# Kernel tuning notes

Measured on AMD Instinct MI355X. Metric: run time of the kernel, lower is better.

Reference implementation:

```python
import jax, jax.numpy as jnp
import numpy as np

B, T, C = 2, 2048, 1024
NH, LAT, DHR = 16, 512, 64
DK = C // NH  # 64


def _rope(x, d):
    # interleaved RoPE as in source: freq = t+1, theta per pair repeated twice
    Tx = x.shape[1]
    freq = jnp.arange(Tx, dtype=jnp.float32)[:, None] + 1.0            # [T,1]
    pos = jnp.arange(d // 2, dtype=jnp.float32)[:, None]
    pos = jnp.repeat(pos, 2, axis=-1).reshape(1, -1)                   # [1,d] -> p0,p0,p1,p1,...
    theta = jnp.exp(-2.0 * pos / d * jnp.log(10000.0))
    cos = jnp.cos(freq * theta)                                        # [T,d]
    sin = jnp.sin(freq * theta)
    x32 = x.astype(jnp.float32)
    x1 = x32[..., 0::2]
    x2 = x32[..., 1::2]
    xrot = jnp.stack([-x2, x1], axis=-1).reshape(x32.shape)
    return (x32 * cos + xrot * sin).astype(x.dtype)


def setup_inputs() -> dict:
    key = jax.random.key(0)
    ks = jax.random.split(key, 13)
    s = lambda k, sh, fan: jax.random.normal(k, sh, jnp.float32) / np.sqrt(fan)
    return {
        'x': jax.random.normal(ks[0], (B, T, C), jnp.float32),
        'w1': s(ks[1], (C, 2 * LAT), C), 'b1': jnp.zeros((2 * LAT,), jnp.float32),
        'wkr': s(ks[2], (2 * LAT, DHR), 2 * LAT), 'bkr': jnp.zeros((DHR,), jnp.float32),
        'wqr': s(ks[3], (2 * LAT, DHR * NH), 2 * LAT), 'bqr': jnp.zeros((DHR * NH,), jnp.float32),
        'wkv': s(ks[4], (LAT, 2 * C), LAT), 'bkv': jnp.zeros((2 * C,), jnp.float32),
        'wq': s(ks[5], (LAT, C), LAT), 'bq': jnp.zeros((C,), jnp.float32),
        'wo': s(ks[6], (C, C), C), 'bo': jnp.zeros((C,), jnp.float32),
    }


def reference(x, w1, b1, wkr, bkr, wqr, bqr, wkv, bkv, wq, bq, wo, bo):
    h = x @ w1 + b1                           # [B,T,2*LAT]
    cKV, cq = jnp.split(h, 2, axis=-1)        # each [B,T,LAT]

    kRt = _rope(h @ wkr + bkr, DHR)           # [B,T,DHR]
    qRt = _rope(h @ wqr + bqr, DHR * NH)      # [B,T,NH*DHR]
    qRt = qRt.reshape(B, T, NH, DHR).transpose(0, 2, 1, 3)  # [B,NH,T,DHR]

    kv = cKV @ wkv + bkv                      # [B,T,2C]
    k, v = jnp.split(kv, 2, axis=-1)
    q = cq @ wq + bq                          # [B,T,C]

    to_heads = lambda t: t.reshape(B, T, NH, DK).transpose(0, 2, 1, 3)
    q, k, v = to_heads(q), to_heads(k), to_heads(v)   # [B,NH,T,DK]

    q = jnp.concatenate([q, qRt], axis=-1)                              # [B,NH,T,DK+DHR]
    kR = jnp.broadcast_to(kRt[:, None, :, :], (B, NH, T, DHR))
    k = jnp.concatenate([k, kR], axis=-1)                               # [B,NH,T,DK+DHR]

    dk = q.shape[-1]
    qf, kf, vf = q.astype(jnp.float32), k.astype(jnp.float32), v.astype(jnp.float32)
    w = jnp.einsum('bnTd,bntd->bnTt', qf, kf) * dk ** (-0.5)            # [B,NH,T,T]
    mask = jnp.tril(jnp.ones((T, T), jnp.float32))
    w = jnp.where(mask == 0, -jnp.inf, w)
    w = jax.nn.softmax(w, axis=-1)
    out = jnp.einsum('bnTt,bntd->bnTd', w, vf).astype(x.dtype)          # [B,NH,T,DK]

    out = out.transpose(0, 2, 1, 3).reshape(B, T, C)
    return out @ wo + bo
```

## Files before the change

### kernel.cpp

```cpp
#include <hip/hip_runtime.h>
#include <math.h>
#include <stdint.h>

#define B_   2
#define T_   2048
#define C_   1024
#define NH_  16
#define LAT_ 512
#define DHR_ 64
#define M_   (B_*T_)

typedef unsigned short u16;
typedef unsigned int u32;
typedef short short8 __attribute__((ext_vector_type(8)));
typedef short short4v __attribute__((ext_vector_type(4)));
typedef float f32x4 __attribute__((ext_vector_type(4)));

#define SCALE2 0.12752455489626498f

__device__ __forceinline__ u16 f2bf(float f) {
    union { float f; unsigned u; } x; x.f = f;
    unsigned r = x.u + 0x7fffu + ((x.u >> 16) & 1u);
    return (u16)(r >> 16);
}
__device__ __forceinline__ float bf2f(u16 v) {
    union { unsigned u; float f; } x; x.u = ((unsigned)v) << 16;
    return x.f;
}
__device__ __forceinline__ u32 asu32(float f) {
    union { float f; u32 u; } x; x.f = f; return x.u;
}
__device__ __forceinline__ u32 pack_bf2(float lo, float hi) {
    u32 a = asu32(lo) + 0x8000u;
    u32 b = asu32(hi) + 0x8000u;
    return __builtin_amdgcn_perm(b, a, 0x07060302u);
}

__device__ __forceinline__ void gl_lds16(const void* g, void* l) {
    auto* gp = reinterpret_cast<const __attribute__((address_space(1))) unsigned*>(
        reinterpret_cast<uintptr_t>(g));
    auto* lp = reinterpret_cast<__attribute__((address_space(3))) unsigned*>(
        reinterpret_cast<uintptr_t>(l));
    __builtin_amdgcn_global_load_lds(gp, lp, 16, 0, 0);
}

__device__ __forceinline__ void tr_tile(const float* __restrict__ W,
                                        u16* __restrict__ Wt,
                                        int K, int N, int bx, int by, int tid,
                                        float (*t)[33])
{
    const int tx = tid & 31;
    const int ty = tid >> 5;
    const int n0 = bx << 5;
    const int k0 = by << 5;
    #pragma unroll
    for (int r = 0; r < 4; ++r) {
        int row = ty + (r << 3);
        t[row][tx] = W[(size_t)(k0 + row) * N + n0 + tx];
    }
    __syncthreads();
    #pragma unroll
    for (int r = 0; r < 4; ++r) {
        int row = ty + (r << 3);
        Wt[(size_t)(n0 + row) * K + k0 + tx] = f2bf(t[tx][row]);
    }
}

__global__ __launch_bounds__(256)
void prep_all(const float* __restrict__ x, u16* __restrict__ xb,
              const float* __restrict__ w1,  const float* __restrict__ wqr,
              const float* __restrict__ wkr, const float* __restrict__ wkv,
              const float* __restrict__ wq,  const float* __restrict__ wo,
              u16* __restrict__ w1t,  u16* __restrict__ wqkt,
              u16* __restrict__ wkvt, u16* __restrict__ wqt,
              u16* __restrict__ wot,
              const float* __restrict__ bqr, const float* __restrict__ bkr,
              float* __restrict__ bqk)
{
    __shared__ float t[32][33];
    int id = blockIdx.x;
    const int tid = threadIdx.x;
    if (id < 4096) {
        int i = id * 256 + tid;
        float4 v = ((const float4*)x)[i];
        short4v s;
        s[0] = f2bf(v.x); s[1] = f2bf(v.y); s[2] = f2bf(v.z); s[3] = f2bf(v.w);
        ((short4v*)xb)[i] = s;
        return;
    }
    id -= 4096;
    if (id < 1024)      { tr_tile(w1,  w1t,  1024, 1024, id % 32, id / 32, tid, t); return; }
    id -= 1024;
    if (id < 1024)      { tr_tile(wqr, wqkt, 1024, 1024, id % 32, id / 32, tid, t); return; }
    id -= 1024;
    if (id < 64)        { tr_tile(wkr, wqkt + 1024 * 1024, 1024, 64, id % 2, id / 2, tid, t); return; }
    id -= 64;
    if (id < 1024)      { tr_tile(wkv, wkvt, 512, 2048, id % 64, id / 64, tid, t); return; }
    id -= 1024;
    if (id < 512)       { tr_tile(wq,  wqt,  512, 1024, id % 32, id / 32, tid, t); return; }
    id -= 512;
    if (id < 1024)      { tr_tile(wo,  wot,  1024, 1024, id % 32, id / 32, tid, t); return; }
    for (int i = tid; i < 1152; i += 256) {
        float v;
        if (i < 1024)      v = bqr[i];
        else if (i < 1088) v = bkr[i - 1024];
        else               v = 0.f;
        bqk[i] = v;
    }
}

template<int BM, int BN>
__device__ __forceinline__ void gemm_body(
    u16* __restrict__ AsB, u16* __restrict__ BsB,
    const u16* __restrict__ A, int lda,
    const u16* __restrict__ Bt, const float* __restrict__ bias,
    void* __restrict__ Out, bool outf32, float oscale,
    int N, int K, int m0, int n0, int tid)
{
    constexpr int MI = BM / 32;
    constexpr int NI = BN / 32;
    const int lane = tid & 63;
    const int ln   = lane & 15;
    const int quad = lane >> 4;
    const int wv   = tid >> 6;
    const int wm   = (wv & 1) * (BM / 2);
    const int wn   = (wv >> 1) * (BN / 2);

    f32x4 acc[MI][NI];
    #pragma unroll
    for (int i = 0; i < MI; ++i)
        #pragma unroll
        for (int j = 0; j < NI; ++j) acc[i][j] = (f32x4){0.f, 0.f, 0.f, 0.f};

    auto stage = [&](int bufi, int k0) {
        u16* As = AsB + bufi * (BM * 32);
        u16* Bs = BsB + bufi * (BN * 32);
        #pragma unroll
        for (int it = 0; it < BM / 64; ++it) {
            int flat = it * 256 + tid;
            gl_lds16(A + (size_t)(m0 + (flat >> 2)) * lda + k0 + ((flat & 3) << 3),
                     &As[flat * 8]);
        }
        #pragma unroll
        for (int it = 0; it < BN / 64; ++it) {
            int flat = it * 256 + tid;
            gl_lds16(Bt + (size_t)(n0 + (flat >> 2)) * K + k0 + ((flat & 3) << 3),
                     &Bs[flat * 8]);
        }
    };

    stage(0, 0);
    __syncthreads();

    int buf = 0;
    for (int k0 = 0; k0 < K; k0 += 32) {
        if (k0 + 32 < K) stage(buf ^ 1, k0 + 32);

        u16* As = AsB + buf * (BM * 32);
        u16* Bs = BsB + buf * (BN * 32);
        short8 af[MI], bfv[NI];
        #pragma unroll
        for (int mi = 0; mi < MI; ++mi)
            af[mi] = *(const short8*)(&As[(wm + mi * 16 + ln) * 32 + quad * 8]);
        #pragma unroll
        for (int ni = 0; ni < NI; ++ni)
            bfv[ni] = *(const short8*)(&Bs[(wn + ni * 16 + ln) * 32 + quad * 8]);
        #pragma unroll
        for (int mi = 0; mi < MI; ++mi)
            #pragma unroll
            for (int ni = 0; ni < NI; ++ni)
                acc[mi][ni] = __builtin_amdgcn_mfma_f32_16x16x32_bf16(af[mi], bfv[ni], acc[mi][ni], 0, 0, 0);

        __syncthreads();
        buf ^= 1;
    }

    float bb[NI];
    #pragma unroll
    for (int ni = 0; ni < NI; ++ni) bb[ni] = bias[n0 + wn + ni * 16 + ln];

    #pragma unroll
    for (int mi = 0; mi < MI; ++mi) {
        #pragma unroll
        for (int r = 0; r < 4; ++r) {
            const size_t row = (size_t)(m0 + wm + mi * 16 + quad * 4 + r);
            #pragma unroll
            for (int ni = 0; ni < NI; ++ni) {
                float v = (acc[mi][ni][r] + bb[ni]) * oscale;
                const size_t idx = row * N + n0 + wn + ni * 16 + ln;
                if (outf32) ((float*)Out)[idx] = v;
                else        ((u16*)Out)[idx]  = f2bf(v);
            }
        }
    }
}

template<int BM, int BN, bool OUTF32>
__global__ __launch_bounds__(256, 4)
void gemm_mfma(const u16* __restrict__ A, int lda,
               const u16* __restrict__ Bt,
               const float* __restrict__ bias,
               void* __restrict__ Out, int N, int K, float oscale)
{
    __shared__ __align__(16) u16 As[2 * BM * 32];
    __shared__ __align__(16) u16 Bs[2 * BN * 32];
    gemm_body<BM, BN>(As, Bs, A, lda, Bt, bias, Out, OUTF32, oscale,
                      N, K, blockIdx.y * BM, blockIdx.x * BN, threadIdx.x);
}

__global__ __launch_bounds__(256, 4)
void gemm3(const u16* __restrict__ hb,
           const u16* __restrict__ wqkt, const float* __restrict__ bqk, u16* __restrict__ Zqk,
           const u16* __restrict__ wkvt, const float* __restrict__ bkv, u16* __restrict__ kvbb,
           const u16* __restrict__ wqt,  const float* __restrict__ bq,  u16* __restrict__ qb)
{
    __shared__ __align__(16) u16 As[2 * 4096];
    __shared__ __align__(16) u16 Bs[2 * 4096];
    int id = blockIdx.x;
    const u16* A; const u16* Bt; const float* bias; u16* Out; int N, K, bx, by;
    float osc = 1.0f;
    if (id < 288)      { A = hb;       Bt = wqkt; bias = bqk; Out = Zqk;  N = 1152; K = 1024; bx = id % 9;  by = id / 9; }
    else if (id < 800) { id -= 288; A = hb;       Bt = wkvt; bias = bkv; Out = kvbb; N = 2048; K = 512;  bx = id % 16; by = id / 16; }
    else               { id -= 800; A = hb + 512; Bt = wqt;  bias = bq;  Out = qb;   N = 1024; K = 512;  bx = id % 8;  by = id / 8; osc = SCALE2; }
    gemm_body<128, 128>(As, Bs, A, 1024, Bt, bias, Out, false, osc, N, K,
                        by * 128, bx * 128, threadIdx.x);
}

__global__ void rope_bf(u16* __restrict__ Zqk)
{
    int idx = blockIdx.x * 256 + threadIdx.x;
    u16* p;
    int t;
    float e, osc;
    if (idx < M_ * 512) {
        int row = idx >> 9, pr = idx & 511;
        e = (-2.0f * (float)pr / 1024.0f) * 9.210340371976184f;
        p = Zqk + (size_t)row * 1152 + (pr << 1);
        t = row & (T_ - 1);
        osc = SCALE2;
    } else {
        int r = idx - M_ * 512;
        if (r >= M_ * 32) return;
        int row = r >> 5, pr = r & 31;
        e = (-2.0f * (float)pr / 64.0f) * 9.210340371976184f;
        p = Zqk + 1024 + (size_t)row * 1152 + (pr << 1);
        t = row & (T_ - 1);
        osc = 1.0f;
    }
    float theta = expf(e);
    float ang = (float)(t + 1) * theta;
    float s = sinf(ang), c = cosf(ang);
    float x1 = bf2f(p[0]);
    float x2 = bf2f(p[1]);
    p[0] = f2bf((x1 * c - x2 * s) * osc);
    p[1] = f2bf((x2 * c + x1 * s) * osc);
}

__global__ __launch_bounds__(256)
void reshape_kv(const u16* __restrict__ kvb,
                const u16* __restrict__ kR, int kRstride,
                u16* __restrict__ Kf,
                u16* __restrict__ Vt)
{
    __shared__ u16 t[64 * 68];
    const int tid = threadIdx.x;
    const int bh  = blockIdx.y;
    const int kt  = blockIdx.x;
    const int b = bh >> 4, h = bh & 15;
    const int bT = b * T_;
    const int k0 = kt << 6;

    #pragma unroll
    for (int it = 0; it < 4; ++it) {
        int flat = it * 256 + tid;
        int j = flat >> 4;
        int g = flat & 15;
        int gl = g ^ (j & 7);
        const u16* src = (g < 8)
            ? (kvb + (size_t)(bT + k0 + j) * 2048 + h * 64 + ((gl & 7) << 3))
            : (kR  + (size_t)(bT + k0 + j) * kRstride + ((gl & 7) << 3));
        *(short8*)(Kf + ((size_t)bh * 2048 + k0 + j) * 128 + (g << 3)) = *(const short8*)src;
    }
    #pragma unroll
    for (int it = 0; it < 2; ++it) {
        int flat = it * 256 + tid;
        int j  = flat >> 3;
        int d8 = (flat & 7) << 3;
        *(short8*)(&t[j * 68 + d8]) =
            *(const short8*)(kvb + (size_t)(bT + k0 + j) * 2048 + 1024 + h * 64 + d8);
    }
    __syncthreads();
    #pragma unroll
    for (int it = 0; it < 2; ++it) {
        int flat = it * 256 + tid;
        int dv = flat >> 3;
        int p  = flat & 7;
        int gl = p ^ (dv & 7);
        short8 v;
        #pragma unroll
        for (int e = 0; e < 8; ++e) v[e] = (short)t[(gl * 8 + e) * 68 + dv];
        *(short8*)(Vt + (size_t)bh * 131072 + (size_t)dv * 2048 + k0 + (p << 3)) = v;
    }
}

__global__ __launch_bounds__(256, 2)
void attn_mfma(const u16* __restrict__ qh,
               const u16* __restrict__ qR, int qRstride,
               const u16* __restrict__ Kf,
               const u16* __restrict__ Vtg,
               u16* __restrict__ Opart,
               float* __restrict__ Lpart)
{
    __shared__ __align__(16) u16 Ks[2][64 * 128];
    __shared__ __align__(16) u16 Vt[2][64 * 64];
    __shared__ __align__(16) u16 Ps[4 * 32 * 64];

    const int tid  = threadIdx.x;
    const int lane = tid & 63;
    const int ln   = lane & 15;
    const int quad = lane >> 4;
    const int wv   = tid >> 6;
    const int bh   = blockIdx.y;
    const int b    = bh >> 4;
    const int h    = bh & 15;
    const int bT   = b * T_;
    const int p    = blockIdx.x & 7;
    const int s    = blockIdx.x >> 3;
    const int ln7  = ln & 7;

    auto stage = [&](int bufi, int kt) {
        const u16* ksrc = Kf + ((size_t)bh * 2048 + (kt << 6)) * 128;
        #pragma unroll
        for (int it = 0; it < 4; ++it) {
            int flat = it * 256 + tid;
            gl_lds16(ksrc + flat * 8, &Ks[bufi][flat * 8]);
        }
        const u16* vsrc = Vtg + (size_t)bh * 131072 + (kt << 6);
        #pragma unroll
        for (int it = 0; it < 2; ++it) {
            int flat = it * 256 + tid;
            gl_lds16(vsrc + (size_t)(flat >> 3) * 2048 + ((flat & 7) << 3),
                     &Vt[bufi][flat * 8]);
        }
    };

    const int qts[2]    = { p, 15 - p };
    const int halves[2] = { s, 1 - s };

    for (int seg = 0; seg < 2; ++seg) {
        const int qt   = qts[seg];
        const int hf   = halves[seg];
        const int n    = 2 * qt + 2;
        const int ktlo = hf ? (n >> 1) : 0;
        const int kthi = hf ? n : (n >> 1);
        const int part = ((bh * 16 + qt) << 1) + hf;
        const int wq0  = qt * 128 + wv * 32;

        short8 aq[2][4];
        #pragma unroll
        for (int ni = 0; ni < 2; ++ni) {
            const size_t row = (size_t)(bT + wq0 + ni * 16 + ln);
            #pragma unroll
            for (int kk = 0; kk < 4; ++kk) {
                const int col = kk * 32 + quad * 8;
                const u16* src = (kk < 2)
                    ? (qh + row * C_ + h * 64 + col)
                    : (qR + row * qRstride + h * 64 + (col - 64));
                aq[ni][kk] = *(const short8*)src;
            }
        }

        f32x4 O[2][4];
        float l_lane[2] = { 0.f, 0.f };
        #pragma unroll
        for (int ni = 0; ni < 2; ++ni)
            #pragma unroll
            for (int mt = 0; mt < 4; ++mt) O[ni][mt] = (f32x4){0.f, 0.f, 0.f, 0.f};

        stage(0, ktlo);
        __syncthreads();

        for (int kt = ktlo; kt < kthi; ++kt) {
            const int cur = (kt - ktlo) & 1;
            if (kt + 1 < kthi) stage(cur ^ 1, kt + 1);

            const int k0 = kt << 6;
            if (k0 <= wq0 + 31) {
                f32x4 S[2][4];
                #pragma unroll
                for (int ni = 0; ni < 2; ++ni)
                    #pragma unroll
                    for (int mi = 0; mi < 4; ++mi)
                        S[ni][mi] = (f32x4){0.f, 0.f, 0.f, 0.f};

                #pragma unroll
                for (int kk = 0; kk < 4; ++kk) {
                    #pragma unroll
                    for (int mi = 0; mi < 4; ++mi) {
                        short8 ak = *(const short8*)(
                            &Ks[cur][(mi * 16 + ln) * 128 + (((kk * 4 + quad) ^ ln7) << 3)]);
                        S[0][mi] = __builtin_amdgcn_mfma_f32_16x16x32_bf16(ak, aq[0][kk], S[0][mi], 0, 0, 0);
                        S[1][mi] = __builtin_amdgcn_mfma_f32_16x16x32_bf16(ak, aq[1][kk], S[1][mi], 0, 0, 0);
                    }
                }

                const bool full = (k0 + 63) <= wq0;

                #pragma unroll
                for (int ni = 0; ni < 2; ++ni) {
                    const int qg = wq0 + ni * 16 + ln;
                    float ll = 0.f;
                    #pragma unroll
                    for (int mi = 0; mi < 4; ++mi) {
                        float pv[4];
                        #pragma unroll
                        for (int r = 0; r < 4; ++r) {
                            float sc = S[ni][mi][r];
                            if (!full) {
                                int key = k0 + mi * 16 + quad * 4 + r;
                                if (key > qg) sc = -1e30f;
                            }
                            pv[r] = __builtin_amdgcn_exp2f(sc);
                        }
                        ll += (pv[0] + pv[1]) + (pv[2] + pv[3]);
                        u32 pk0 = pack_bf2(pv[0], pv[1]);
                        u32 pk1 = pack_bf2(pv[2], pv[3]);
                        u32* dst = (u32*)&Ps[(wv * 32 + ni * 16 + ln) * 64 +
                                             (((mi * 2 + (quad >> 1)) ^ ln7) << 3) +
                                             ((quad & 1) << 2)];
                        dst[0] = pk0;
                        dst[1] = pk1;
                    }
                    l_lane[ni] += ll;
                }

                asm volatile("s_waitcnt lgkmcnt(0)" ::: "memory");

                #pragma unroll
                for (int c = 0; c < 2; ++c) {
                    const int pos = ((c * 4 + quad) ^ ln7) << 3;
                    short8 pb0 = *(const short8*)(&Ps[(wv * 32 +  0 + ln) * 64 + pos]);
                    short8 pb1 = *(const short8*)(&Ps[(wv * 32 + 16 + ln) * 64 + pos]);
                    #pragma unroll
                    for (int mt = 0; mt < 4; ++mt) {
                        short8 av = *(const short8*)(&Vt[cur][(mt * 16 + ln) * 64 + pos]);
                        O[0][mt] = __builtin_amdgcn_mfma_f32_16x16x32_bf16(av, pb0, O[0][mt], 0, 0, 0);
                        O[1][mt] = __builtin_amdgcn_mfma_f32_16x16x32_bf16(av, pb1, O[1][mt], 0, 0, 0);
                    }
                }
            }
            __syncthreads();
        }

        #pragma unroll
        for (int ni = 0; ni < 2; ++ni) {
            float l = l_lane[ni];
            l += __shfl_xor(l, 16);
            l += __shfl_xor(l, 32);
            const int qlocal = wv * 32 + ni * 16 + ln;
            u16* dst = Opart + ((size_t)part * 128 + qlocal) * 64;
            #pragma unroll
            for (int mt = 0; mt < 4; ++mt) {
                short4v o;
                o[0] = (short)f2bf(O[ni][mt][0]);
                o[1] = (short)f2bf(O[ni][mt][1]);
                o[2] = (short)f2bf(O[ni][mt][2]);
                o[3] = (short)f2bf(O[ni][mt][3]);
                *(short4v*)(dst + mt * 16 + quad * 4) = o;
            }
            if (quad == 0)
                Lpart[part * 128 + qlocal] = l;
            l_lane[ni] = 0.f;
        }
    }
}

__global__ void attn_merge(const u16* __restrict__ Opart,
                           const float* __restrict__ Lpart,
                           u16* __restrict__ out)
{
    int g = blockIdx.x * 256 + threadIdx.x;
    int row    = g >> 4;
    int c4     = (g & 15) << 2;
    int bhqt   = row >> 7;
    int qlocal = row & 127;
    float l0 = Lpart[(bhqt << 1) * 128 + qlocal];
    float l1 = Lpart[((bhqt << 1) + 1) * 128 + qlocal];
    float inv = 1.0f / (l0 + l1);
    short4v s0 = *(const short4v*)(Opart + ((size_t)(bhqt << 1) * 128 + qlocal) * 64 + c4);
    short4v s1 = *(const short4v*)(Opart + ((size_t)((bhqt << 1) + 1) * 128 + qlocal) * 64 + c4);
    int bh = bhqt >> 4, qt = bhqt & 15;
    int b = bh >> 4, h = bh & 15;
    size_t orow = (size_t)(b * T_ + qt * 128 + qlocal);
    short4v o;
    o[0] = (short)f2bf((bf2f((u16)s0[0]) + bf2f((u16)s1[0])) * inv);
    o[1] = (short)f2bf((bf2f((u16)s0[1]) + bf2f((u16)s1[1])) * inv);
    o[2] = (short)f2bf((bf2f((u16)s0[2]) + bf2f((u16)s1[2])) * inv);
    o[3] = (short)f2bf((bf2f((u16)s0[3]) + bf2f((u16)s1[3])) * inv);
    *(short4v*)(out + orow * C_ + h * 64 + c4) = o;
}

extern "C" void kernel_launch(void* const* d_in, const int* in_sizes, int n_in,
                              void* d_out, int out_size, void* d_ws, size_t ws_size,
                              hipStream_t stream)
{
    const float* x   = (const float*)d_in[0];
    const float* w1  = (const float*)d_in[1];
    const float* b1  = (const float*)d_in[2];
    const float* wkr = (const float*)d_in[3];
    const float* bkr = (const float*)d_in[4];
    const float* wqr = (const float*)d_in[5];
    const float* bqr = (const float*)d_in[6];
    const float* wkv = (const float*)d_in[7];
    const float* bkv = (const float*)d_in[8];
    const float* wq  = (const float*)d_in[9];
    const float* bq  = (const float*)d_in[10];
    const float* wo  = (const float*)d_in[11];
    const float* bo  = (const float*)d_in[12];
    float* out = (float*)d_out;

    u16* ws    = (u16*)d_ws;
    u16* buf0  = ws;
    u16* buf1  = buf0 + 4194304;
    u16* Zqk   = buf1 + 4194304;
    u16* kvbb  = Zqk  + 4718592;
    u16* w1t   = kvbb + 8388608;
    u16* wqkt  = w1t  + 1048576;
    u16* wkvt  = wqkt + 1179648;
    u16* wqt   = wkvt + 1048576;
    u16* wot   = wqt  + 524288;
    float* bqk = (float*)(wot + 1048576);
    u16* Kf    = (u16*)(bqk + 1280);
    u16* Vtg   = Kf  + 8388608;
    u16* Opart = Vtg + 4194304;
    float* Lprt = (float*)(Opart + 8388608);

    u16* xb    = buf0;
    u16* qb    = buf0;
    u16* hb    = buf1;
    u16* attnb = buf1;

    dim3 blk(256);

    prep_all<<<8769, blk, 0, stream>>>(x, xb, w1, wqr, wkr, wkv, wq, wo,
                                       w1t, wqkt, wkvt, wqt, wot,
                                       bqr, bkr, bqk);

    gemm_mfma<128, 64, false><<<dim3(16, 32), blk, 0, stream>>>(xb, 1024, w1t, b1, hb, 1024, 1024, 1.0f);
    gemm3<<<1056, blk, 0, stream>>>(hb, wqkt, bqk, Zqk, wkvt, bkv, kvbb, wqt, bq, qb);
    rope_bf<<<(M_ * 544 + 255) / 256, blk, 0, stream>>>(Zqk);
    reshape_kv<<<dim3(32, 32), blk, 0, stream>>>(kvbb, Zqk + 1024, 1152, Kf, Vtg);
    attn_mfma<<<dim3(16, 32), blk, 0, stream>>>(qb, Zqk, 1152, Kf, Vtg, Opart, Lprt);
    attn_merge<<<4096, blk, 0, stream>>>(Opart, Lprt, attnb);
    gemm_mfma<128, 64, true><<<dim3(16, 32), blk, 0, stream>>>(attnb, 1024, wot, bo, out, 1024, 1024, 1.0f);
}
```

Baseline: 240.8 us.

## Split attention key range into thirds and single-buffer K/V tiles

```diff
diff --git a/kernel.cpp b/kernel.cpp
--- a/kernel.cpp
+++ b/kernel.cpp
@@ -196,7 +196,7 @@
 }
 
 template<int BM, int BN, bool OUTF32>
-__global__ __launch_bounds__(256, 4)
+__global__ __launch_bounds__(256, 3)
 void gemm_mfma(const u16* __restrict__ A, int lda,
                const u16* __restrict__ Bt,
                const float* __restrict__ bias,
@@ -208,7 +208,7 @@
                       N, K, blockIdx.y * BM, blockIdx.x * BN, threadIdx.x);
 }
 
-__global__ __launch_bounds__(256, 4)
+__global__ __launch_bounds__(256, 3)
 void gemm3(const u16* __restrict__ hb,
            const u16* __restrict__ wqkt, const float* __restrict__ bqk, u16* __restrict__ Zqk,
            const u16* __restrict__ wkvt, const float* __restrict__ bkv, u16* __restrict__ kvbb,
@@ -303,7 +303,7 @@
     }
 }
 
-__global__ __launch_bounds__(256, 2)
+__global__ __launch_bounds__(256, 3)
 void attn_mfma(const u16* __restrict__ qh,
                const u16* __restrict__ qR, int qRstride,
                const u16* __restrict__ Kf,
@@ -311,8 +311,8 @@
                u16* __restrict__ Opart,
                float* __restrict__ Lpart)
 {
-    __shared__ __align__(16) u16 Ks[2][64 * 128];
-    __shared__ __align__(16) u16 Vt[2][64 * 64];
+    __shared__ __align__(16) u16 Ks[64 * 128];
+    __shared__ __align__(16) u16 Vt[64 * 64];
     __shared__ __align__(16) u16 Ps[4 * 32 * 64];
 
     const int tid  = threadIdx.x;
@@ -324,51 +324,37 @@
     const int b    = bh >> 4;
     const int h    = bh & 15;
     const int bT   = b * T_;
-    const int p    = blockIdx.x & 7;
-    const int s    = blockIdx.x >> 3;
+    const int p    = blockIdx.x / 3;
+    const int a    = blockIdx.x % 3;
     const int ln7  = ln & 7;
 
-    auto stage = [&](int bufi, int kt) {
+    auto stage = [&](int kt) {
         const u16* ksrc = Kf + ((size_t)bh * 2048 + (kt << 6)) * 128;
         #pragma unroll
         for (int it = 0; it < 4; ++it) {
             int flat = it * 256 + tid;
-            gl_lds16(ksrc + flat * 8, &Ks[bufi][flat * 8]);
+            gl_lds16(ksrc + flat * 8, &Ks[flat * 8]);
         }
         const u16* vsrc = Vtg + (size_t)bh * 131072 + (kt << 6);
         #pragma unroll
         for (int it = 0; it < 2; ++it) {
             int flat = it * 256 + tid;
             gl_lds16(vsrc + (size_t)(flat >> 3) * 2048 + ((flat & 7) << 3),
-                     &Vt[bufi][flat * 8]);
+                     &Vt[flat * 8]);
         }
     };
 
     const int qts[2]    = { p, 15 - p };
-    const int halves[2] = { s, 1 - s };
+    const int thirds[2] = { a, 2 - a };
 
     for (int seg = 0; seg < 2; ++seg) {
         const int qt   = qts[seg];
-        const int hf   = halves[seg];
+        const int th   = thirds[seg];
         const int n    = 2 * qt + 2;
-        const int ktlo = hf ? (n >> 1) : 0;
-        const int kthi = hf ? n : (n >> 1);
-        const int part = ((bh * 16 + qt) << 1) + hf;
+        const int ktlo = th * n / 3;
+        const int kthi = (th + 1) * n / 3;
+        const int part = (bh * 16 + qt) * 3 + th;
         const int wq0  = qt * 128 + wv * 32;
-
-        short8 aq[2][4];
-        #pragma unroll
-        for (int ni = 0; ni < 2; ++ni) {
-            const size_t row = (size_t)(bT + wq0 + ni * 16 + ln);
-            #pragma unroll
-            for (int kk = 0; kk < 4; ++kk) {
-                const int col = kk * 32 + quad * 8;
-                const u16* src = (kk < 2)
-                    ? (qh + row * C_ + h * 64 + col)
-                    : (qR + row * qRstride + h * 64 + (col - 64));
-                aq[ni][kk] = *(const short8*)src;
-            }
-        }
 
         f32x4 O[2][4];
         float l_lane[2] = { 0.f, 0.f };
@@ -377,79 +363,92 @@
             #pragma unroll
             for (int mt = 0; mt < 4; ++mt) O[ni][mt] = (f32x4){0.f, 0.f, 0.f, 0.f};
 
-        stage(0, ktlo);
-        __syncthreads();
-
-        for (int kt = ktlo; kt < kthi; ++kt) {
-            const int cur = (kt - ktlo) & 1;
-            if (kt + 1 < kthi) stage(cur ^ 1, kt + 1);
-
-            const int k0 = kt << 6;
-            if (k0 <= wq0 + 31) {
-                f32x4 S[2][4];
-                #pragma unroll
-                for (int ni = 0; ni < 2; ++ni)
-                    #pragma unroll
-                    for (int mi = 0; mi < 4; ++mi)
-                        S[ni][mi] = (f32x4){0.f, 0.f, 0.f, 0.f};
-
+        if (ktlo < kthi) {
+            short8 aq[2][4];
+            #pragma unroll
+            for (int ni = 0; ni < 2; ++ni) {
+                const size_t row = (size_t)(bT + wq0 + ni * 16 + ln);
                 #pragma unroll
                 for (int kk = 0; kk < 4; ++kk) {
+                    const int col = kk * 32 + quad * 8;
+                    const u16* src = (kk < 2)
+                        ? (qh + row * C_ + h * 64 + col)
+                        : (qR + row * qRstride + h * 64 + (col - 64));
+                    aq[ni][kk] = *(const short8*)src;
+                }
+            }
+
+            for (int kt = ktlo; kt < kthi; ++kt) {
+                __syncthreads();
+                stage(kt);
+                __syncthreads();
+
+                const int k0 = kt << 6;
+                if (k0 <= wq0 + 31) {
+                    f32x4 S[2][4];
                     #pragma unroll
-                    for (int mi = 0; mi < 4; ++mi) {
-                        short8 ak = *(const short8*)(
-                            &Ks[cur][(mi * 16 + ln) * 128 + (((kk * 4 + quad) ^ ln7) << 3)]);
-                        S[0][mi] = __builtin_amdgcn_mfma_f32_16x16x32_bf16(ak, aq[0][kk], S[0][mi], 0, 0, 0);
-                        S[1][mi] = __builtin_amdgcn_mfma_f32_16x16x32_bf16(ak, aq[1][kk], S[1][mi], 0, 0, 0);
+                    for (int ni = 0; ni < 2; ++ni)
+                        #pragma unroll
+                        for (int mi = 0; mi < 4; ++mi)
+                            S[ni][mi] = (f32x4){0.f, 0.f, 0.f, 0.f};
+
+                    #pragma unroll
+                    for (int kk = 0; kk < 4; ++kk) {
+                        #pragma unroll
+                        for (int mi = 0; mi < 4; ++mi) {
+                            short8 ak = *(const short8*)(
+                                &Ks[(mi * 16 + ln) * 128 + (((kk * 4 + quad) ^ ln7) << 3)]);
+                            S[0][mi] = __builtin_amdgcn_mfma_f32_16x16x32_bf16(ak, aq[0][kk], S[0][mi], 0, 0, 0);
+                            S[1][mi] = __builtin_amdgcn_mfma_f32_16x16x32_bf16(ak, aq[1][kk], S[1][mi], 0, 0, 0);
+                        }
                     }
-                }
-
-                const bool full = (k0 + 63) <= wq0;
-
-                #pragma unroll
-                for (int ni = 0; ni < 2; ++ni) {
-                    const int qg = wq0 + ni * 16 + ln;
-                    float ll = 0.f;
+
+                    const bool full = (k0 + 63) <= wq0;
+
                     #pragma unroll
-                    for (int mi = 0; mi < 4; ++mi) {
-                        float pv[4];
+                    for (int ni = 0; ni < 2; ++ni) {
+                        const int qg = wq0 + ni * 16 + ln;
+                        float ll = 0.f;
                         #pragma unroll
-                        for (int r = 0; r < 4; ++r) {
-                            float sc = S[ni][mi][r];
-                            if (!full) {
-                                int key = k0 + mi * 16 + quad * 4 + r;
-                                if (key > qg) sc = -1e30f;
+                        for (int mi = 0; mi < 4; ++mi) {
+                            float pv[4];
+                            #pragma unroll
+                            for (int r = 0; r < 4; ++r) {
+                                float sc = S[ni][mi][r];
+                                if (!full) {
+                                    int key = k0 + mi * 16 + quad * 4 + r;
+                                    if (key > qg) sc = -1e30f;
+                                }
+                                pv[r] = __builtin_amdgcn_exp2f(sc);
                             }
-                            pv[r] = __builtin_amdgcn_exp2f(sc);
+                            ll += (pv[0] + pv[1]) + (pv[2] + pv[3]);
+                            u32 pk0 = pack_bf2(pv[0], pv[1]);
+                            u32 pk1 = pack_bf2(pv[2], pv[3]);
+                            u32* dst = (u32*)&Ps[(wv * 32 + ni * 16 + ln) * 64 +
+                                                 (((mi * 2 + (quad >> 1)) ^ ln7) << 3) +
+                                                 ((quad & 1) << 2)];
+                            dst[0] = pk0;
+                            dst[1] = pk1;
                         }
-                        ll += (pv[0] + pv[1]) + (pv[2] + pv[3]);
-                        u32 pk0 = pack_bf2(pv[0], pv[1]);
-                        u32 pk1 = pack_bf2(pv[2], pv[3]);
-                        u32* dst = (u32*)&Ps[(wv * 32 + ni * 16 + ln) * 64 +
-                                             (((mi * 2 + (quad >> 1)) ^ ln7) << 3) +
-                                             ((quad & 1) << 2)];
-                        dst[0] = pk0;
-                        dst[1] = pk1;
+                        l_lane[ni] += ll;
                     }
-                    l_lane[ni] += ll;
-                }
-
-                asm volatile("s_waitcnt lgkmcnt(0)" ::: "memory");
-
-                #pragma unroll
-                for (int c = 0; c < 2; ++c) {
-                    const int pos = ((c * 4 + quad) ^ ln7) << 3;
-                    short8 pb0 = *(const short8*)(&Ps[(wv * 32 +  0 + ln) * 64 + pos]);
-                    short8 pb1 = *(const short8*)(&Ps[(wv * 32 + 16 + ln) * 64 + pos]);
+
+                    asm volatile("s_waitcnt lgkmcnt(0)" ::: "memory");
+
                     #pragma unroll
-                    for (int mt = 0; mt < 4; ++mt) {
-                        short8 av = *(const short8*)(&Vt[cur][(mt * 16 + ln) * 64 + pos]);
-                        O[0][mt] = __builtin_amdgcn_mfma_f32_16x16x32_bf16(av, pb0, O[0][mt], 0, 0, 0);
-                        O[1][mt] = __builtin_amdgcn_mfma_f32_16x16x32_bf16(av, pb1, O[1][mt], 0, 0, 0);
+                    for (int c = 0; c < 2; ++c) {
+                        const int pos = ((c * 4 + quad) ^ ln7) << 3;
+                        short8 pb0 = *(const short8*)(&Ps[(wv * 32 +  0 + ln) * 64 + pos]);
+                        short8 pb1 = *(const short8*)(&Ps[(wv * 32 + 16 + ln) * 64 + pos]);
+                        #pragma unroll
+                        for (int mt = 0; mt < 4; ++mt) {
+                            short8 av = *(const short8*)(&Vt[(mt * 16 + ln) * 64 + pos]);
+                            O[0][mt] = __builtin_amdgcn_mfma_f32_16x16x32_bf16(av, pb0, O[0][mt], 0, 0, 0);
+                            O[1][mt] = __builtin_amdgcn_mfma_f32_16x16x32_bf16(av, pb1, O[1][mt], 0, 0, 0);
+                        }
                     }
                 }
             }
-            __syncthreads();
         }
 
         #pragma unroll
@@ -470,7 +469,6 @@
             }
             if (quad == 0)
                 Lpart[part * 128 + qlocal] = l;
-            l_lane[ni] = 0.f;
         }
     }
 }
@@ -484,19 +482,22 @@
     int c4     = (g & 15) << 2;
     int bhqt   = row >> 7;
     int qlocal = row & 127;
-    float l0 = Lpart[(bhqt << 1) * 128 + qlocal];
-    float l1 = Lpart[((bhqt << 1) + 1) * 128 + qlocal];
-    float inv = 1.0f / (l0 + l1);
-    short4v s0 = *(const short4v*)(Opart + ((size_t)(bhqt << 1) * 128 + qlocal) * 64 + c4);
-    short4v s1 = *(const short4v*)(Opart + ((size_t)((bhqt << 1) + 1) * 128 + qlocal) * 64 + c4);
+    int base   = bhqt * 3;
+    float l = Lpart[(base + 0) * 128 + qlocal]
+            + Lpart[(base + 1) * 128 + qlocal]
+            + Lpart[(base + 2) * 128 + qlocal];
+    float inv = 1.0f / l;
+    short4v s0 = *(const short4v*)(Opart + ((size_t)(base + 0) * 128 + qlocal) * 64 + c4);
+    short4v s1 = *(const short4v*)(Opart + ((size_t)(base + 1) * 128 + qlocal) * 64 + c4);
+    short4v s2 = *(const short4v*)(Opart + ((size_t)(base + 2) * 128 + qlocal) * 64 + c4);
     int bh = bhqt >> 4, qt = bhqt & 15;
     int b = bh >> 4, h = bh & 15;
     size_t orow = (size_t)(b * T_ + qt * 128 + qlocal);
     short4v o;
-    o[0] = (short)f2bf((bf2f((u16)s0[0]) + bf2f((u16)s1[0])) * inv);
-    o[1] = (short)f2bf((bf2f((u16)s0[1]) + bf2f((u16)s1[1])) * inv);
-    o[2] = (short)f2bf((bf2f((u16)s0[2]) + bf2f((u16)s1[2])) * inv);
-    o[3] = (short)f2bf((bf2f((u16)s0[3]) + bf2f((u16)s1[3])) * inv);
+    o[0] = (short)f2bf((bf2f((u16)s0[0]) + bf2f((u16)s1[0]) + bf2f((u16)s2[0])) * inv);
+    o[1] = (short)f2bf((bf2f((u16)s0[1]) + bf2f((u16)s1[1]) + bf2f((u16)s2[1])) * inv);
+    o[2] = (short)f2bf((bf2f((u16)s0[2]) + bf2f((u16)s1[2]) + bf2f((u16)s2[2])) * inv);
+    o[3] = (short)f2bf((bf2f((u16)s0[3]) + bf2f((u16)s1[3]) + bf2f((u16)s2[3])) * inv);
     *(short4v*)(out + orow * C_ + h * 64 + c4) = o;
 }
 
@@ -520,23 +521,23 @@
     float* out = (float*)d_out;
 
     u16* ws    = (u16*)d_ws;
-    u16* buf0  = ws;
-    u16* buf1  = buf0 + 4194304;
-    u16* Zqk   = buf1 + 4194304;
-    u16* kvbb  = Zqk  + 4718592;
-    u16* w1t   = kvbb + 8388608;
-    u16* wqkt  = w1t  + 1048576;
-    u16* wkvt  = wqkt + 1179648;
-    u16* wqt   = wkvt + 1048576;
-    u16* wot   = wqt  + 524288;
-    float* bqk = (float*)(wot + 1048576);
-    u16* Kf    = (u16*)(bqk + 1280);
-    u16* Vtg   = Kf  + 8388608;
-    u16* Opart = Vtg + 4194304;
-    float* Lprt = (float*)(Opart + 8388608);
-
-    u16* xb    = buf0;
-    u16* qb    = buf0;
+    u16* xb    = ws;
+    u16* kvbb  = ws + 4194304;
+    u16* w1t   = ws + 12582912;
+    u16* buf1  = ws + 13631488;
+    u16* qb    = ws + 17825792;
+    u16* Zqk   = ws + 22020096;
+    u16* wqkt  = ws + 26738688;
+    u16* wkvt  = ws + 27918336;
+    u16* wqt   = ws + 28966912;
+    u16* wot   = ws + 29491200;
+    float* bqk = (float*)(ws + 30539776);
+    u16* Kf    = ws + 30542336;
+    u16* Vtg   = ws + 38930944;
+
+    u16* Opart  = ws;
+    float* Lprt = (float*)w1t;
+
     u16* hb    = buf1;
     u16* attnb = buf1;
 
@@ -550,7 +551,7 @@
     gemm3<<<1056, blk, 0, stream>>>(hb, wqkt, bqk, Zqk, wkvt, bkv, kvbb, wqt, bq, qb);
     rope_bf<<<(M_ * 544 + 255) / 256, blk, 0, stream>>>(Zqk);
     reshape_kv<<<dim3(32, 32), blk, 0, stream>>>(kvbb, Zqk + 1024, 1152, Kf, Vtg);
-    attn_mfma<<<dim3(16, 32), blk, 0, stream>>>(qb, Zqk, 1152, Kf, Vtg, Opart, Lprt);
+    attn_mfma<<<dim3(24, 32), blk, 0, stream>>>(qb, Zqk, 1152, Kf, Vtg, Opart, Lprt);
     attn_merge<<<4096, blk, 0, stream>>>(Opart, Lprt, attnb);
     gemm_mfma<128, 64, true><<<dim3(16, 32), blk, 0, stream>>>(attnb, 1024, wot, bo, out, 1024, 1024, 1.0f);
 }
```

Measured after the change: 241.0 us. About the same (+0.1%).
